# Kernel optimization log

Measured on AMD Instinct MI355X. Metric: run time of the kernel, lower is better.

Reference implementation:

```python
import jax, jax.numpy as jnp
import numpy as np

N_EMBED = 1024
N_HEAD = 16
D = N_EMBED // N_HEAD
B, T = 2, 2048
EPS = 1e-5


def _layer_norm(x, w, b):
    mu = jnp.mean(x, axis=-1, keepdims=True)
    var = jnp.mean(jnp.square(x - mu), axis=-1, keepdims=True)
    return (x - mu) * jax.lax.rsqrt(var + EPS) * w + b


def setup_inputs() -> dict:
    key = jax.random.key(0)
    ks = jax.random.split(key, 13)
    E = N_EMBED
    s_attn = 1.0 / np.sqrt(E)
    s_fc = 1.0 / np.sqrt(E)
    s_proj = 1.0 / np.sqrt(4 * E)
    return {
        "x": jax.random.normal(ks[0], (B, T, E), jnp.float32),
        "ln1_w": jnp.ones((E,), jnp.float32),
        "ln1_b": jnp.ones((E,), jnp.float32),
        "w_qkv": jax.random.normal(ks[1], (E, 3 * E), jnp.float32) * s_attn,
        "b_qkv": jax.random.normal(ks[2], (3 * E,), jnp.float32) * 0.02,
        "w_o": jax.random.normal(ks[3], (E, E), jnp.float32) * s_attn,
        "b_o": jax.random.normal(ks[4], (E,), jnp.float32) * 0.02,
        "ln2_w": jnp.ones((E,), jnp.float32),
        "ln2_b": jnp.ones((E,), jnp.float32),
        "w_fc": jax.random.normal(ks[5], (E, 4 * E), jnp.float32) * s_fc,
        "b_fc": jax.random.normal(ks[6], (4 * E,), jnp.float32) * 0.02,
        "w_proj": jax.random.normal(ks[7], (4 * E, E), jnp.float32) * s_proj,
        "b_proj": jax.random.normal(ks[8], (E,), jnp.float32) * 0.02,
    }


def reference(x, ln1_w, ln1_b, w_qkv, b_qkv, w_o, b_o, ln2_w, ln2_b, w_fc, b_fc, w_proj, b_proj):
    Bb, Tt, E = x.shape
    # --- attention branch ---
    h = _layer_norm(x, ln1_w, ln1_b)
    qkv = h @ w_qkv + b_qkv                         # [B,T,3E]
    q, k, v = jnp.split(qkv, 3, axis=-1)
    q = q.reshape(Bb, Tt, N_HEAD, D).transpose(0, 2, 1, 3)  # [B,H,T,D]
    k = k.reshape(Bb, Tt, N_HEAD, D).transpose(0, 2, 1, 3)
    v = v.reshape(Bb, Tt, N_HEAD, D).transpose(0, 2, 1, 3)
    scale = 1.0 / np.sqrt(D)
    a = scale * jnp.einsum("bhqd,bhkd->bhqk", q, k)  # [B,H,T,T]
    causal = jnp.tril(jnp.ones((Tt, Tt), bool))
    a = jnp.where(causal, a, -jnp.inf)
    a = jax.nn.softmax(a, axis=-1)
    y = jnp.einsum("bhqk,bhkd->bhqd", a, v)          # [B,H,T,D]
    y = y.transpose(0, 2, 1, 3).reshape(Bb, Tt, E)
    y = y @ w_o + b_o
    x = x + y
    # --- MLP branch ---
    h = _layer_norm(x, ln2_w, ln2_b)
    h = jax.nn.gelu(h @ w_fc + b_fc, approximate=False)
    h = h @ w_proj + b_proj
    return x + h
```

## Files before the change

### kernel.cpp

```cpp
#include <hip/hip_runtime.h>
#include <cstdint>
#include <cstddef>

#define E 1024
#define TT 2048
#define NB 2
#define NH 16
#define HD 64

using u16 = unsigned short;
using bf16x8 = __attribute__((ext_vector_type(8))) __bf16;
using floatx4 = __attribute__((ext_vector_type(4))) float;
using s16x4 = __attribute__((ext_vector_type(4))) short;

__device__ __forceinline__ float b2f(u16 u) {
  unsigned int x = ((unsigned int)u) << 16;
  float f;
  __builtin_memcpy(&f, &x, 4);
  return f;
}
__device__ __forceinline__ u16 f2b(float f) {
  unsigned int x;
  __builtin_memcpy(&x, &f, 4);
  x += 0x7fffu + ((x >> 16) & 1u);
  return (u16)(x >> 16);
}
__device__ __forceinline__ u16 f2b_fast(float f) {
  unsigned int x;
  float g = f * 1.001953125f;
  __builtin_memcpy(&x, &g, 4);
  return (u16)(x >> 16);
}

__device__ __forceinline__ void async16(const u16* g, u16* l) {
  __builtin_amdgcn_global_load_lds(
      (const __attribute__((address_space(1))) unsigned int*)g,
      (__attribute__((address_space(3))) unsigned int*)l, 16, 0, 0);
}

__device__ __forceinline__ floatx4 mfma32(bf16x8 a, bf16x8 b, floatx4 c) {
  return __builtin_amdgcn_mfma_f32_16x16x32_bf16(a, b, c, 0, 0, 0);
}

__device__ __forceinline__ floatx4 mfma16(s16x4 a, s16x4 b, floatx4 c) {
#if defined(__HIP_DEVICE_COMPILE__)
  return __builtin_amdgcn_mfma_f32_16x16x16bf16_1k(a, b, c, 0, 0, 0);
#else
  return c;
#endif
}

__global__ __launch_bounds__(256) void wconv_all(
    const float* __restrict__ w0, const float* __restrict__ w1,
    const float* __restrict__ w2, const float* __restrict__ w3,
    u16* __restrict__ o0, u16* __restrict__ o1, u16* __restrict__ o2,
    u16* __restrict__ o3) {
  __shared__ float tile[32][33];
  const int t = blockIdx.x;
  const float* w;
  u16* o;
  int K, N, nx, ti;
  if (t < 3072) { w = w0; o = o0; K = 1024; N = 3072; nx = 96; ti = t; }
  else if (t < 4096) { w = w1; o = o1; K = 1024; N = 1024; nx = 32; ti = t - 3072; }
  else if (t < 8192) { w = w2; o = o2; K = 1024; N = 4096; nx = 128; ti = t - 4096; }
  else { w = w3; o = o3; K = 4096; N = 1024; nx = 32; ti = t - 8192; }
  const int n0 = (ti % nx) * 32, k0 = (ti / nx) * 32;
  const int tx = threadIdx.x, ty = threadIdx.y;
#pragma unroll
  for (int i = 0; i < 32; i += 8)
    tile[ty + i][tx] = w[(size_t)(k0 + ty + i) * N + (n0 + tx)];
  __syncthreads();
#pragma unroll
  for (int i = 0; i < 32; i += 8)
    o[(size_t)(n0 + ty + i) * K + (k0 + tx)] = f2b(tile[tx][ty + i]);
}

__global__ __launch_bounds__(256) void ln_kernel(const float* __restrict__ x,
                                                 const float* __restrict__ w,
                                                 const float* __restrict__ bvec,
                                                 u16* __restrict__ outb) {
  const int row = blockIdx.x;
  const int t = threadIdx.x;
  const float4 v = ((const float4*)(x + (size_t)row * E))[t];
  float s1 = v.x + v.y + v.z + v.w;
  float s2 = v.x * v.x + v.y * v.y + v.z * v.z + v.w * v.w;
#pragma unroll
  for (int off = 32; off > 0; off >>= 1) {
    s1 += __shfl_down(s1, off);
    s2 += __shfl_down(s2, off);
  }
  __shared__ float r1[4], r2[4];
  if ((t & 63) == 0) { r1[t >> 6] = s1; r2[t >> 6] = s2; }
  __syncthreads();
  s1 = r1[0] + r1[1] + r1[2] + r1[3];
  s2 = r2[0] + r2[1] + r2[2] + r2[3];
  const float mean = s1 * (1.f / E);
  const float var = s2 * (1.f / E) - mean * mean;
  const float rstd = rsqrtf(var + 1e-5f);
  const float4 wv = ((const float4*)w)[t];
  const float4 bv = ((const float4*)bvec)[t];
  const u16 o0 = f2b((v.x - mean) * rstd * wv.x + bv.x);
  const u16 o1 = f2b((v.y - mean) * rstd * wv.y + bv.y);
  const u16 o2 = f2b((v.z - mean) * rstd * wv.z + bv.z);
  const u16 o3 = f2b((v.w - mean) * rstd * wv.w + bv.w);
  uint2 pk;
  pk.x = (unsigned)o0 | ((unsigned)o1 << 16);
  pk.y = (unsigned)o2 | ((unsigned)o3 << 16);
  ((uint2*)(outb + (size_t)row * E))[t] = pk;
}

template <int MODE, int ROWS>
__global__ __launch_bounds__(512) void gemm_bt(const u16* __restrict__ A,
                                               const u16* __restrict__ BT,
                                               const float* __restrict__ bias,
                                               const float* __restrict__ res,
                                               void* __restrict__ outp,
                                               int M, int N, int K) {
  constexpr int NJ = (ROWS == 256) ? 4 : 2;
  __shared__ __align__(16) u16 As[2][ROWS * 32];
  __shared__ __align__(16) u16 Bs[2][128 * 32];
  const int tid = threadIdx.x;
  const int wave = tid >> 6, lane = tid & 63;

  const int gx = gridDim.x, gy = gridDim.y;
  const int L = blockIdx.y * gx + blockIdx.x;
  const int xc = L & 7, wi = L >> 3;
  const int cpg = gx >> 2;
  const int rpg = gy >> 1;
  const int bxs = (xc >> 1) * cpg + (wi % cpg);
  const int bys = (xc & 1) * rpg + (wi / cpg);

  const int row0 = bys * ROWS, col0 = bxs * 128;
  const int wm = (ROWS == 256) ? (wave & 3) * 64 : (wave & 1) * 64;
  const int wn = (ROWS == 256) ? (wave >> 2) * 64 : (wave >> 1) * 32;
  const int r = lane & 15, qd = lane >> 4;

  floatx4 acc[4][NJ];
#pragma unroll
  for (int i = 0; i < 4; i++)
#pragma unroll
    for (int j = 0; j < NJ; j++) acc[i][j] = (floatx4){0.f, 0.f, 0.f, 0.f};

  const int cA0 = tid, cA1 = tid + 512, cB = tid;
  const u16* ApA = A + (size_t)(row0 + (cA0 >> 2)) * K + (cA0 & 3) * 8;
  const u16* ApB = A + (size_t)(row0 + (cA1 >> 2)) * K + (cA1 & 3) * 8;
  const u16* Bp = BT + (size_t)(col0 + (cB >> 2)) * K + (cB & 3) * 8;

  auto stage = [&](int kt, u16* Asb, u16* Bsb) {
    async16(ApA + kt, Asb + cA0 * 8);
    if (ROWS == 256) async16(ApB + kt, Asb + cA1 * 8);
    async16(Bp + kt, Bsb + cB * 8);
  };
  auto compute = [&](const u16* Asb, const u16* Bsb) {
    bf16x8 af[4], bfr[NJ];
#pragma unroll
    for (int i = 0; i < 4; i++)
      af[i] = *(const bf16x8*)&Asb[(wm + i * 16 + r) * 32 + qd * 8];
#pragma unroll
    for (int j = 0; j < NJ; j++)
      bfr[j] = *(const bf16x8*)&Bsb[(wn + j * 16 + r) * 32 + qd * 8];
#pragma unroll
    for (int i = 0; i < 4; i++)
#pragma unroll
      for (int j = 0; j < NJ; j++)
        acc[i][j] = mfma32(af[i], bfr[j], acc[i][j]);
  };

  const int nIter = K >> 5;
  stage(0, As[0], Bs[0]);
  for (int t = 0; t < nIter; t++) {
    const int tb = t & 1;
    if (t + 1 < nIter) {
      stage((t + 1) * 32, As[tb ^ 1], Bs[tb ^ 1]);
      if (ROWS == 256)
        asm volatile("s_waitcnt vmcnt(3)" ::: "memory");
      else
        asm volatile("s_waitcnt vmcnt(2)" ::: "memory");
    } else {
      asm volatile("s_waitcnt vmcnt(0)" ::: "memory");
    }
    asm volatile("s_barrier" ::: "memory");
    compute(As[tb], Bs[tb]);
    asm volatile("s_barrier" ::: "memory");
  }

#pragma unroll
  for (int i = 0; i < 4; i++) {
#pragma unroll
    for (int j = 0; j < NJ; j++) {
      const int col = col0 + wn + j * 16 + r;
      const float bc = bias[col];
      if (MODE == 3) {
        u16* base = (u16*)outp;
        const int rowb = row0 + wm + i * 16 + qd * 4;
        if (col < 2048) {
          const size_t cb =
              (col < 1024) ? (size_t)col : ((size_t)4096 * 1024 + (col - 1024));
#pragma unroll
          for (int rr = 0; rr < 4; rr++)
            base[cb + (size_t)(rowb + rr) * 1024] = f2b(acc[i][j][rr] + bc);
        } else {
          ushort4 pk;
          pk.x = f2b(acc[i][j][0] + bc);
          pk.y = f2b(acc[i][j][1] + bc);
          pk.z = f2b(acc[i][j][2] + bc);
          pk.w = f2b(acc[i][j][3] + bc);
          *(ushort4*)(base + (size_t)8 * 1024 * 1024 +
                      (size_t)(col - 2048) * 4096 + rowb) = pk;
        }
      } else {
#pragma unroll
        for (int rr = 0; rr < 4; rr++) {
          const int row = row0 + wm + i * 16 + qd * 4 + rr;
          const float v = acc[i][j][rr] + bc;
          const size_t idx = (size_t)row * N + col;
          if (MODE == 0) {
            ((u16*)outp)[idx] = f2b(v);
          } else if (MODE == 1) {
            ((float*)outp)[idx] = v + res[idx];
          } else {
            const float z = 1.5957691216f * v * (1.f + 0.044715f * v * v);
            const float g = v / (1.f + __expf(-z));
            ((u16*)outp)[idx] = f2b(g);
          }
        }
      }
    }
  }
}

__global__ __launch_bounds__(256, 2) void attn_mfma(const u16* __restrict__ qb,
                                                    const u16* __restrict__ kb,
                                                    const u16* __restrict__ vtb,
                                                    u16* __restrict__ y) {
  const int bx = blockIdx.x;
  const int h = blockIdx.y, b = blockIdx.z;
  const int qt = b ? (15 - bx) : bx;
  const int tid = threadIdx.x;
  const int wave = tid >> 6, lane = tid & 63;
  const int quad = lane >> 4, r = lane & 15;

  __shared__ __align__(16) u16 Ks[2][128 * 64];
  __shared__ __align__(16) u16 Vs[2][64 * 128];

  const float C = 0.125f * 1.44269504f;
  const int qbase = qt * 128 + wave * 32;

  bf16x8 qf[2][2];
#pragma unroll
  for (int f = 0; f < 2; f++) {
    const u16* qp = qb + ((size_t)b * TT + qbase + f * 16 + r) * E + h * 64;
#pragma unroll
    for (int kh = 0; kh < 2; kh++) {
      union { bf16x8 v; u16 u[8]; } tmp;
#pragma unroll
      for (int j = 0; j < 8; j++) tmp.u[j] = f2b(b2f(qp[kh * 32 + quad * 8 + j]) * C);
      qf[f][kh] = tmp.v;
    }
  }

  floatx4 o[2][4];
#pragma unroll
  for (int f = 0; f < 2; f++)
#pragma unroll
    for (int i = 0; i < 4; i++) o[f][i] = (floatx4){0.f, 0.f, 0.f, 0.f};
  float lsum[2] = {0.f, 0.f};
  const bool mgt[4] = {(quad * 4 + 0) > r, (quad * 4 + 1) > r,
                       (quad * 4 + 2) > r, (quad * 4 + 3) > r};

  auto stageKV = [&](int it, int bi) {
    const int k0 = it * 128;
#pragma unroll
    for (int i = 0; i < 4; i++) {
      const int c = tid + i * 256;
      const int key = c >> 3, dc = (c & 7) ^ (key & 7);
      async16(kb + ((size_t)b * TT + k0 + key) * E + h * 64 + dc * 8, &Ks[bi][c * 8]);
    }
#pragma unroll
    for (int i = 0; i < 4; i++) {
      const int c = tid + i * 256;
      const int d = c >> 4, kc = (c & 15) ^ (d & 15);
      async16(vtb + (size_t)(h * 64 + d) * (NB * TT) + b * TT + k0 + kc * 8,
              &Vs[bi][c * 8]);
    }
  };

  const int nIter = qt + 1;
  stageKV(0, 0);
  for (int it = 0; it < nIter; it++) {
    if (it + 1 < nIter) {
      stageKV(it + 1, (it + 1) & 1);
      asm volatile("s_waitcnt vmcnt(8)" ::: "memory");
    } else {
      asm volatile("s_waitcnt vmcnt(0)" ::: "memory");
    }
    asm volatile("s_barrier" ::: "memory");
    const u16* Kb = Ks[it & 1];
    const u16* Vb = Vs[it & 1];
    const int k0 = it * 128;
    const int relA = (qbase - k0) >> 4;
    const int kTop = (relA + 1 < 7) ? (relA + 1) : 7;

    floatx4 s[2][8];
#pragma unroll
    for (int ks = 0; ks < 8; ks++) {
      if (ks <= kTop) {
        const int key = ks * 16 + r, kx = key & 7;
        const bf16x8 kf0 = *(const bf16x8*)&Kb[key * 64 + (quad ^ kx) * 8];
        const bf16x8 kf1 = *(const bf16x8*)&Kb[key * 64 + ((4 + quad) ^ kx) * 8];
        floatx4 a0 = (floatx4){0.f, 0.f, 0.f, 0.f};
        a0 = mfma32(kf0, qf[0][0], a0);
        a0 = mfma32(kf1, qf[0][1], a0);
        s[0][ks] = a0;
        floatx4 a1 = (floatx4){0.f, 0.f, 0.f, 0.f};
        a1 = mfma32(kf0, qf[1][0], a1);
        a1 = mfma32(kf1, qf[1][1], a1);
        s[1][ks] = a1;
      }
    }

#pragma unroll
    for (int ks = 0; ks < 8; ks++) {
      if (ks <= kTop) {
        s16x4 vf[4];
#pragma unroll
        for (int dsub = 0; dsub < 4; dsub++) {
          const int d = dsub * 16 + r;
          vf[dsub] = *(const s16x4*)&Vb[d * 128 + ((2 * ks + (quad >> 1)) ^ r) * 8 +
                                        (quad & 1) * 4];
        }
#pragma unroll
        for (int f = 0; f < 2; f++) {
          const int rel = relA + f;
          if (ks <= rel) {
            float p0 = exp2f(s[f][ks][0]);
            float p1 = exp2f(s[f][ks][1]);
            float p2 = exp2f(s[f][ks][2]);
            float p3 = exp2f(s[f][ks][3]);
            if (ks == rel) {
              if (mgt[0]) p0 = 0.f;
              if (mgt[1]) p1 = 0.f;
              if (mgt[2]) p2 = 0.f;
              if (mgt[3]) p3 = 0.f;
            }
            lsum[f] += p0 + p1 + p2 + p3;
            s16x4 pk;
            pk[0] = (short)f2b_fast(p0);
            pk[1] = (short)f2b_fast(p1);
            pk[2] = (short)f2b_fast(p2);
            pk[3] = (short)f2b_fast(p3);
#pragma unroll
            for (int dsub = 0; dsub < 4; dsub++)
              o[f][dsub] = mfma16(pk, vf[dsub], o[f][dsub]);
          }
        }
      }
    }
    asm volatile("s_barrier" ::: "memory");
  }

#pragma unroll
  for (int f = 0; f < 2; f++) {
    float lv = lsum[f];
    lv += __shfl_xor(lv, 16);
    lv += __shfl_xor(lv, 32);
#pragma unroll
    for (int rr = 0; rr < 4; rr++) {
      const float linv = 1.f / __shfl(lv, quad * 4 + rr);
      const size_t row = (size_t)b * TT + qbase + f * 16 + quad * 4 + rr;
#pragma unroll
      for (int dsub = 0; dsub < 4; dsub++)
        y[row * E + h * 64 + dsub * 16 + r] = f2b(o[f][dsub][rr] * linv);
    }
  }
}

extern "C" void kernel_launch(void* const* d_in, const int* in_sizes, int n_in,
                              void* d_out, int out_size, void* d_ws, size_t ws_size,
                              hipStream_t stream) {
  (void)in_sizes; (void)n_in; (void)out_size; (void)ws_size;
  const float* x      = (const float*)d_in[0];
  const float* ln1w   = (const float*)d_in[1];
  const float* ln1b   = (const float*)d_in[2];
  const float* w_qkv  = (const float*)d_in[3];
  const float* b_qkv  = (const float*)d_in[4];
  const float* w_o    = (const float*)d_in[5];
  const float* b_o    = (const float*)d_in[6];
  const float* ln2w   = (const float*)d_in[7];
  const float* ln2b   = (const float*)d_in[8];
  const float* w_fc   = (const float*)d_in[9];
  const float* b_fc   = (const float*)d_in[10];
  const float* w_proj = (const float*)d_in[11];
  const float* b_proj = (const float*)d_in[12];
  float* out = (float*)d_out;

  char* p = (char*)d_ws;
  u16* wT_qkv  = (u16*)p; p += (size_t)3072 * 1024 * 2;
  u16* wT_o    = (u16*)p; p += (size_t)1024 * 1024 * 2;
  u16* wT_fc   = (u16*)p; p += (size_t)4096 * 1024 * 2;
  u16* wT_proj = (u16*)p; p += (size_t)1024 * 4096 * 2;
  u16* hbuf    = (u16*)p; p += (size_t)4096 * 1024 * 2;
  u16* qkvb    = (u16*)p; p += (size_t)4096 * 3072 * 2;
  float* x2    = (float*)p; p += (size_t)4096 * 1024 * 4;
  u16* gbuf    = (u16*)p; p += (size_t)4096 * 4096 * 2;

  u16* qb  = qkvb;
  u16* kb  = qkvb + (size_t)4096 * 1024;
  u16* vtb = qkvb + (size_t)8 * 1024 * 1024;

  wconv_all<<<12288, dim3(32, 8), 0, stream>>>(w_qkv, w_o, w_fc, w_proj,
                                               wT_qkv, wT_o, wT_fc, wT_proj);

  ln_kernel<<<4096, 256, 0, stream>>>(x, ln1w, ln1b, hbuf);
  gemm_bt<3, 256><<<dim3(3072 / 128, 4096 / 256), 512, 0, stream>>>(
      hbuf, wT_qkv, b_qkv, nullptr, qkvb, 4096, 3072, 1024);
  attn_mfma<<<dim3(16, NH, NB), 256, 0, stream>>>(qb, kb, vtb, hbuf);
  gemm_bt<1, 128><<<dim3(1024 / 128, 4096 / 128), 512, 0, stream>>>(
      hbuf, wT_o, b_o, x, x2, 4096, 1024, 1024);
  ln_kernel<<<4096, 256, 0, stream>>>(x2, ln2w, ln2b, hbuf);
  gemm_bt<2, 256><<<dim3(4096 / 128, 4096 / 256), 512, 0, stream>>>(
      hbuf, wT_fc, b_fc, nullptr, gbuf, 4096, 4096, 1024);
  gemm_bt<1, 128><<<dim3(1024 / 128, 4096 / 128), 512, 0, stream>>>(
      gbuf, wT_proj, b_proj, x2, out, 4096, 1024, 4096);
}
```

Before: 361.6 us.

## Add intra-block split-K GEMM with 4-stage async pipeline for residual projections

Adds a new GEMM kernel for the two N=1024 residual-output projections (attention output and MLP down-projection). Its 8 waves split into two K-groups that each compute half of every 64-wide K step on a 128x128 tile, then reduce through shared memory before the bias and residual epilogue. It also uses a 4-deep async-copy ring buffer with explicit vmcnt waits and a block-index swizzle for cache locality. The aim is more waves in flight per output tile and better latency hiding on these narrow GEMMs, at the cost of a shared-memory reduction and higher LDS use.

```diff
diff --git a/kernel.cpp b/kernel.cpp
--- a/kernel.cpp
+++ b/kernel.cpp
@@ -223,6 +223,112 @@
             const float g = v / (1.f + __expf(-z));
             ((u16*)outp)[idx] = f2b(g);
           }
+        }
+      }
+    }
+  }
+}
+
+__global__ __launch_bounds__(512) void gemm_ks(const u16* __restrict__ A,
+                                               const u16* __restrict__ BT,
+                                               const float* __restrict__ bias,
+                                               const float* __restrict__ res,
+                                               float* __restrict__ outp,
+                                               int M, int N, int K) {
+  __shared__ __align__(16) u16 As[4][2][128 * 32];
+  __shared__ __align__(16) u16 Bs[4][2][128 * 32];
+  const int tid = threadIdx.x;
+  const int wave = tid >> 6, lane = tid & 63;
+
+  const int gx = gridDim.x, gy = gridDim.y;
+  const int L = blockIdx.y * gx + blockIdx.x;
+  const int xc = L & 7, wi = L >> 3;
+  const int cpg = gx >> 2, rpg = gy >> 1;
+  const int bxs = (xc >> 1) * cpg + (wi % cpg);
+  const int bys = (xc & 1) * rpg + (wi / cpg);
+
+  const int row0 = bys * 128, col0 = bxs * 128;
+  const int kg = wave >> 2;
+  const int wm = (wave & 1) * 64, wn = ((wave >> 1) & 1) * 64;
+  const int r = lane & 15, qd = lane >> 4;
+
+  floatx4 acc[4][4];
+#pragma unroll
+  for (int i = 0; i < 4; i++)
+#pragma unroll
+    for (int j = 0; j < 4; j++) acc[i][j] = (floatx4){0.f, 0.f, 0.f, 0.f};
+
+  const int arow = tid >> 2, aslot = (tid & 3) * 8;
+  const u16* Ap = A + (size_t)(row0 + arow) * K + aslot;
+  const u16* Bp = BT + (size_t)(col0 + arow) * K + aslot;
+
+  auto stage = [&](int s, int d) {
+    const int k0 = s * 64;
+    async16(Ap + k0, &As[d][0][tid * 8]);
+    async16(Ap + k0 + 32, &As[d][1][tid * 8]);
+    async16(Bp + k0, &Bs[d][0][tid * 8]);
+    async16(Bp + k0 + 32, &Bs[d][1][tid * 8]);
+  };
+  auto compute = [&](int d) {
+    bf16x8 af[4], bfr[4];
+#pragma unroll
+    for (int i = 0; i < 4; i++)
+      af[i] = *(const bf16x8*)&As[d][kg][(wm + i * 16 + r) * 32 + qd * 8];
+#pragma unroll
+    for (int j = 0; j < 4; j++)
+      bfr[j] = *(const bf16x8*)&Bs[d][kg][(wn + j * 16 + r) * 32 + qd * 8];
+#pragma unroll
+    for (int i = 0; i < 4; i++)
+#pragma unroll
+      for (int j = 0; j < 4; j++)
+        acc[i][j] = mfma32(af[i], bfr[j], acc[i][j]);
+  };
+
+  const int nT = K >> 6;
+  stage(0, 0);
+  stage(1, 1);
+  stage(2, 2);
+  for (int tt = 0; tt < nT; tt += 4) {
+#pragma unroll
+    for (int d = 0; d < 4; d++) {
+      const int t = tt + d;
+      const int rem = nT - 1 - t;
+      if (rem >= 2)
+        asm volatile("s_waitcnt vmcnt(8)" ::: "memory");
+      else if (rem == 1)
+        asm volatile("s_waitcnt vmcnt(4)" ::: "memory");
+      else
+        asm volatile("s_waitcnt vmcnt(0)" ::: "memory");
+      asm volatile("s_barrier" ::: "memory");
+      if (t + 3 < nT) stage(t + 3, (d + 3) & 3);
+      compute(d);
+    }
+  }
+
+  __syncthreads();
+  float* S = (float*)&As[0][0][0];
+  const int p = wave & 3;
+  floatx4* W = (floatx4*)S + p * 1024 + lane;
+  if (kg == 1) {
+#pragma unroll
+    for (int i = 0; i < 4; i++)
+#pragma unroll
+      for (int j = 0; j < 4; j++) W[(i * 4 + j) * 64] = acc[i][j];
+  }
+  __syncthreads();
+  if (kg == 0) {
+#pragma unroll
+    for (int i = 0; i < 4; i++) {
+#pragma unroll
+      for (int j = 0; j < 4; j++) {
+        const floatx4 w2 = W[(i * 4 + j) * 64];
+        const int col = col0 + wn + j * 16 + r;
+        const float bc = bias[col];
+#pragma unroll
+        for (int rr = 0; rr < 4; rr++) {
+          const int row = row0 + wm + i * 16 + qd * 4 + rr;
+          const size_t idx = (size_t)row * N + col;
+          outp[idx] = acc[i][j][rr] + w2[rr] + bc + res[idx];
         }
       }
     }
@@ -415,11 +521,11 @@
   gemm_bt<3, 256><<<dim3(3072 / 128, 4096 / 256), 512, 0, stream>>>(
       hbuf, wT_qkv, b_qkv, nullptr, qkvb, 4096, 3072, 1024);
   attn_mfma<<<dim3(16, NH, NB), 256, 0, stream>>>(qb, kb, vtb, hbuf);
-  gemm_bt<1, 128><<<dim3(1024 / 128, 4096 / 128), 512, 0, stream>>>(
+  gemm_ks<<<dim3(1024 / 128, 4096 / 128), 512, 0, stream>>>(
       hbuf, wT_o, b_o, x, x2, 4096, 1024, 1024);
   ln_kernel<<<4096, 256, 0, stream>>>(x2, ln2w, ln2b, hbuf);
   gemm_bt<2, 256><<<dim3(4096 / 128, 4096 / 256), 512, 0, stream>>>(
       hbuf, wT_fc, b_fc, nullptr, gbuf, 4096, 4096, 1024);
-  gemm_bt<1, 128><<<dim3(1024 / 128, 4096 / 128), 512, 0, stream>>>(
+  gemm_ks<<<dim3(1024 / 128, 4096 / 128), 512, 0, stream>>>(
       gbuf, wT_proj, b_proj, x2, out, 4096, 1024, 4096);
 }
```

Measured after the change: 341.1 us. -5.7%, faster.
